# Kernel tuning notes

Hardware: AMD Instinct MI355X
Metric: run time of the kernel (lower is better)

Reference implementation:

```python
import jax, jax.numpy as jnp
import numpy as np

N = 4096          # residues (2 chains x 2048)
CHAINS = 2
LMAX = 2
L = (LMAX + 1) ** 2            # 9 spherical coefficients
BBC = 32                       # bb_channels
NBB = 3                        # n_bb_atoms - 1
SPH = BBC + NBB                # 35 sphere channels fed to attention
KNN = 20
LRK = 40
HEADS = 8
HC = 32
VC = HC // 4                   # attn_value_channels = 8
EDGE_F = 32                    # 16 RBF + 16 positional
L_IDX = np.repeat(np.arange(LMAX + 1), 2 * np.arange(LMAX + 1) + 1)  # degree of each of the 9 coeffs


def so3_linear(x, w, b):
    # x: [N,L,Cin]; w: [LMAX+1,Cin,Cout] shared across m within each degree l; bias only on l=0
    out = jnp.einsum('nlc,lcd->nld', x, w[L_IDX])
    return out.at[:, 0, :].add(b)


def _rbf(d):
    mu = jnp.linspace(0.0, 20.0, 16)
    sigma = 20.0 / 16
    return jnp.exp(-(((d[..., None] - mu) / sigma) ** 2))


def _edge_pos_embed(src, dst):
    d = (src - dst).astype(jnp.float32)
    freq = jnp.exp(jnp.arange(0, 16, 2, dtype=jnp.float32) * (-np.log(10000.0) / 16))
    ang = d[:, None] * freq
    return jnp.concatenate([jnp.cos(ang), jnp.sin(ang)], axis=-1)


def setup_inputs():
    key = jax.random.key(0)
    ks = jax.random.split(key, 16)
    n = lambda i, shp, s=1.0: jax.random.normal(ks[i], shp) * s
    return {
        'X_ca': n(0, (N, 3), 10.0),
        'bb_rel': n(1, (N, NBB, 3)),
        'bb_features': n(2, (N, L, BBC)),
        'batch': jnp.repeat(jnp.arange(CHAINS), N // CHAINS),
        'x_mask': jax.random.uniform(ks[3], (N,)) < 0.02,
        'noising_mask': jax.random.uniform(ks[4], (N,)) < 0.5,
        'attn_w1': n(5, (2 * SPH + EDGE_F, HC), 0.05), 'attn_b1': jnp.zeros((HC,)),
        'attn_w2': n(6, (HC, HEADS), 0.05), 'attn_b2': jnp.zeros((HEADS,)),
        'wv': n(7, (LMAX + 1, SPH, HEADS * VC), 0.05), 'bv': jnp.zeros((HEADS * VC,)),
        'wo': n(8, (LMAX + 1, HEADS * VC, BBC), 0.05), 'bo': jnp.zeros((BBC,)),
        'wg': n(9, (BBC, BBC), 0.05), 'bg': jnp.zeros((BBC,)),
        'wf': n(10, (LMAX + 1, BBC, BBC), 0.05), 'bf': jnp.zeros((BBC,)),
        'w_xca': n(11, (LMAX + 1, BBC, 1), 0.05), 'b_xca': jnp.zeros((1,)),
        'w_gate': n(12, (BBC, 1), 0.05), 'b_gate': jnp.zeros((1,)),
        'w_bb': n(13, (LMAX + 1, BBC, NBB), 0.05), 'b_bb': jnp.zeros((NBB,)),
    }


def reference(X_ca, bb_rel, bb_features, batch, x_mask, noising_mask,
              attn_w1, attn_b1, attn_w2, attn_b2, wv, bv, wo, bo, wg, bg, wf, bf,
              w_xca, b_xca, w_gate, b_gate, w_bb, b_bb):
    Nn = X_ca.shape[0]
    BIG = jnp.float32(1e30)
    # ---- graph construction (knn_graph + sample_inv_cubic_edges) ----
    x2 = jnp.sum(X_ca * X_ca, axis=-1)
    D2 = jnp.maximum(x2[:, None] + x2[None, :] - 2.0 * (X_ca @ X_ca.T), 0.0)  # [N,N]
    same = batch[:, None] == batch[None, :]
    eye = jnp.eye(Nn, dtype=bool)
    mask_pair = x_mask[:, None] | x_mask[None, :]
    invalid = (~same) | eye | mask_pair
    knn_idx = jax.lax.top_k(-jnp.where(invalid, BIG, D2), KNN)[1]   # [N,KNN] sources per target
    # long-range: inverse-cubic distance weights, Gumbel top-k sampling, excluding knn picks
    logits = jnp.where(invalid, -BIG, -1.5 * jnp.log(D2 + 1e-6))
    rows = jnp.arange(Nn)[:, None]
    logits = logits.at[rows, knn_idx].set(-BIG)
    gumb = jax.random.gumbel(jax.random.key(1), (Nn, Nn))
    lr_idx = jax.lax.top_k(logits + gumb, LRK)[1]                   # [N,LRK]
    src = jnp.concatenate([knn_idx.reshape(-1), lr_idx.reshape(-1)])
    dst = jnp.concatenate([jnp.repeat(jnp.arange(Nn), KNN), jnp.repeat(jnp.arange(Nn), LRK)])
    # ---- edge features: RBF(dist) + relative positional embedding ----
    dvec = X_ca[src] - X_ca[dst]
    dist = jnp.linalg.norm(dvec, axis=-1)
    edge_feat = jnp.concatenate([_rbf(dist), _edge_pos_embed(src, dst)], axis=-1)  # [M,32]
    # ---- assemble SO3 node embedding [N,L,35] ----
    node = jnp.zeros((Nn, L, SPH), X_ca.dtype)
    node = node.at[:, :, :BBC].set(bb_features)
    node = node.at[:, 1:4, BBC:].set(jnp.swapaxes(bb_rel, -1, -2))  # l=1 coeffs carry bb_rel
    node = node.at[:, 0, SPH - 1].set(noising_mask.astype(X_ca.dtype))
    # ---- equivariant graph attention (simplified TransBlockV2) ----
    inv = node[:, 0, :]                                             # invariant (l=0) features
    a_in = jnp.concatenate([inv[src], inv[dst], edge_feat], axis=-1)
    h = jax.nn.silu(a_in @ attn_w1 + attn_b1)
    logit = h @ attn_w2 + attn_b2                                   # [M,HEADS]
    mx = jax.ops.segment_max(logit, dst, num_segments=Nn)
    p = jnp.exp(logit - mx[dst])
    Z = jax.ops.segment_sum(p, dst, num_segments=Nn)
    alpha = p / (Z[dst] + 1e-9)                                     # segment softmax per target/head
    v = so3_linear(node, wv, bv)[src].reshape(-1, L, HEADS, VC)     # gather source values
    msg = (v * alpha[:, None, :, None]).reshape(-1, L, HEADS * VC)
    agg = jax.ops.segment_sum(msg, dst, num_segments=Nn)            # scatter to targets
    out = so3_linear(agg, wo, bo)                                   # [N,L,32]
    gate = jax.nn.silu(out[:, 0, :] @ wg + bg)                      # invariant-gated FFN
    out = out + so3_linear(out, wf, bf) * gate[:, None, :]
    # ---- coordinate / backbone updates ----
    upd_x = so3_linear(out, w_xca, b_xca)                           # [N,L,1]
    vec = upd_x[:, 1:4, 0]                                          # l=1 -> 3-vector
    g2 = jax.nn.softplus(out[:, 0, :] @ w_gate + b_gate)            # [N,1]
    new_X = X_ca + jnp.where(noising_mask[:, None], vec * g2, 0.0)
    upd_bb = so3_linear(out, w_bb, b_bb)                            # [N,L,3]
    dbb = jnp.swapaxes(upd_bb[:, 1:4, :], -1, -2)                   # [N,3,3]
    new_bb = bb_rel + jnp.where(noising_mask[:, None, None], dbb, 0.0)
    return new_X, new_bb, out
```

## Files before the change

kernel.cpp:

```cpp
#include <hip/hip_runtime.h>
#include <hip/hip_bf16.h>
#include <stdint.h>

#define NN 4096
#define CS 2048
#define KNN 20
#define LRK 40
#define EPN 60
#define NE (NN*EPN)
#define SPHC 35
#define BBCC 32
#define NHEAD 8
#define HVD 64
#define HCD 32
#define LT 9
#define MAXC 384

#define INVAL_D2 0xFFFFFFFEu
#define CONSUMED 0xFFFFFFFFu

__device__ __forceinline__ float fast_exp(float x) {
  return __builtin_amdgcn_exp2f(x * 1.4426950408889634f);
}
__device__ __forceinline__ float fast_cos(float a) {
  float rev = a * 0.15915494309189535f;
  rev = rev - __builtin_rintf(rev);
  return __builtin_amdgcn_cosf(rev);
}
__device__ __forceinline__ float fast_sin(float a) {
  float rev = a * 0.15915494309189535f;
  rev = rev - __builtin_rintf(rev);
  return __builtin_amdgcn_sinf(rev);
}

__device__ __forceinline__ float neglogu_f(int i, int j) {
  uint32_t c = ((uint32_t)(i & 2047) << 12) | (uint32_t)j;
  const uint32_t ks0 = 0u, ks1 = 1u, ks2 = 0x1BD11BDBu;
  uint32_t x0 = c + ks0;
  uint32_t x1 = (c + 0x800000u) + ks1;
#define TF_R(r) { x0 += x1; x1 = (x1 << (r)) | (x1 >> (32 - (r))); x1 ^= x0; }
  TF_R(13) TF_R(15) TF_R(26) TF_R(6)   x0 += ks1; x1 += ks2 + 1u;
  TF_R(17) TF_R(29) TF_R(16) TF_R(24)  x0 += ks2; x1 += ks0 + 2u;
  TF_R(13) TF_R(15) TF_R(26) TF_R(6)   x0 += ks0; x1 += ks1 + 3u;
  TF_R(17) TF_R(29) TF_R(16) TF_R(24)  x0 += ks1; x1 += ks2 + 4u;
  TF_R(13) TF_R(15) TF_R(26) TF_R(6)   x0 += ks2; x1 += ks0 + 5u;
#undef TF_R
  uint32_t b = (i >= 2048) ? x1 : x0;
  float u = __uint_as_float((b >> 9) | 0x3F800000u) - 1.0f;
  u = u + 1.17549435e-38f;
  return -logf(u);
}

__global__ void prep_kernel(const float* __restrict__ X,
                            const int* __restrict__ batch,
                            const int* __restrict__ xmask,
                            float4* __restrict__ Xw, uint32_t* __restrict__ bm) {
#pragma clang fp contract(off)
  int n = blockIdx.x * blockDim.x + threadIdx.x;
  if (n >= NN) return;
  float x = X[n*3+0], y = X[n*3+1], z = X[n*3+2];
  float x2 = (x*x + y*y) + z*z;
  Xw[n] = make_float4(x, y, z, x2);
  bm[n] = ((uint32_t)batch[n] << 1) | (xmask[n] ? 1u : 0u);
}

__global__ __launch_bounds__(256) void nodeproj_kernel(const float* __restrict__ bbf,
                                                       const int* __restrict__ nmask,
                                                       const float* __restrict__ w1,
                                                       const float* __restrict__ b1,
                                                       float* __restrict__ Pn,
                                                       float* __restrict__ Pd) {
  int tid = threadIdx.x;
  int t = tid & 31;
  int n = blockIdx.x * 8 + (tid >> 5);
  float bv_ = bbf[(size_t)n * (LT*BBCC) + t];
  float an = 0.f, ad = b1[t];
  #pragma unroll 8
  for (int c = 0; c < BBCC; c++) {
    float bc = __shfl(bv_, (tid & 32) + c, 64);
    an = fmaf(bc, w1[c * HCD + t], an);
    ad = fmaf(bc, w1[(SPHC + c) * HCD + t], ad);
  }
  float nm = nmask[n] ? 1.f : 0.f;
  an = fmaf(nm, w1[34 * HCD + t], an);
  ad = fmaf(nm, w1[69 * HCD + t], ad);
  Pn[n * HCD + t] = an;
  Pd[n * HCD + t] = ad;
}

__device__ __forceinline__ void sel2l(uint32_t* val, uint32_t* hist2,
                                      uint32_t* candk, uint32_t* candp,
                                      uint32_t* sh, int* sel,
                                      int k, int base, int cb, int tid) {
  {
    uint4* h4 = (uint4*)hist2;
    uint4 z; z.x = 0; z.y = 0; z.z = 0; z.w = 0;
    h4[tid] = z; h4[tid + 256] = z;
  }
  if (tid == 0) { sh[2] = 0; sh[3] = 0; }
  __syncthreads();
  #pragma unroll
  for (int q = 0; q < 8; q++) {
    uint32_t key = val[tid + (q << 8)];
    atomicAdd(&hist2[key >> 21], 1u);
  }
  __syncthreads();
  uint32_t h[8], s = 0;
  #pragma unroll
  for (int q = 0; q < 8; q++) { h[q] = hist2[tid*8 + q]; s += h[q]; }
  uint32_t cum = s;
  #pragma unroll
  for (int off = 1; off < 64; off <<= 1) {
    uint32_t o = __shfl_up(cum, off, 64);
    if ((tid & 63) >= off) cum += o;
  }
  if ((tid & 63) == 63) sh[8 + (tid >> 6)] = cum;
  __syncthreads();
  uint32_t woff = 0;
  for (int w = 0; w < (tid >> 6); w++) woff += sh[8 + w];
  uint32_t cumAll = cum + woff;
  uint32_t cumBefore = cumAll - s;
  uint32_t rk = (uint32_t)k;
  if (rk > cumBefore && rk <= cumAll) {
    uint32_t rloc = rk - cumBefore, lp = 0;
    bool done = false;
    #pragma unroll
    for (int q = 0; q < 8; q++) {
      lp += h[q];
      if (!done && rloc <= lp) { sh[0] = (uint32_t)(tid*8 + q); sh[1] = rloc - (lp - h[q]); done = true; }
    }
  }
  __syncthreads();
  const uint32_t B = sh[0], r = sh[1];
  #pragma unroll
  for (int q = 0; q < 8; q++) {
    int pos = tid + (q << 8);
    uint32_t key = val[pos];
    if ((key >> 21) == B) {
      uint32_t idx = atomicAdd(&sh[2], 1u);
      if (idx < MAXC) { candk[idx] = key; candp[idx] = (uint32_t)pos; }
    }
  }
  __syncthreads();
  int m = (int)sh[2]; if (m > MAXC) m = MAXC;
  if (tid < 64) {
    for (int ci = tid; ci < m; ci += 64) {
      unsigned long long k64 = ((unsigned long long)candk[ci] << 32) | candp[ci];
      uint32_t rank = 0;
      for (int j = 0; j < m; j++) {
        unsigned long long o = ((unsigned long long)candk[j] << 32) | candp[j];
        rank += (o < k64) ? 1u : 0u;
      }
      if (rank == r - 1) { sh[0] = candk[ci]; sh[1] = candp[ci]; }
    }
  }
  __syncthreads();
  const uint32_t vstar = sh[0], istar = sh[1];
  #pragma unroll
  for (int q = 0; q < 8; q++) {
    int pos = tid + (q << 8);
    uint32_t key = val[pos];
    if (key < vstar || (key == vstar && (uint32_t)pos <= istar)) {
      uint32_t slot = atomicAdd(&sh[3], 1u);
      sel[base + (int)slot] = cb + pos;
    }
  }
  __syncthreads();
}

__global__ __launch_bounds__(256) void select_kernel(const float4* __restrict__ Xw,
                                                     const uint32_t* __restrict__ bm,
                                                     int* __restrict__ srcO) {
#pragma clang fp contract(off)
  __shared__ uint32_t val[CS];
  __shared__ uint32_t hist2[2048];
  __shared__ uint32_t candk[MAXC];
  __shared__ uint32_t candp[MAXC];
  __shared__ uint32_t sh[12];
  __shared__ int sel[EPN];
  const int i = blockIdx.x, tid = threadIdx.x;
  const uint32_t bmi = bm[i];

  if (bmi & 1u) {
    if (tid < KNN) srcO[(size_t)i * EPN + tid] = tid;
    else if (tid < EPN) srcO[(size_t)i * EPN + tid] = tid - KNN;
    return;
  }
  const int cb = (int)(bmi >> 1) * CS;
  const float4 xi = Xw[i];

  #pragma unroll
  for (int q = 0; q < 8; q++) {
    int pos = tid + (q << 8);
    int j = cb + pos;
    float4 xj = Xw[j];
    uint32_t bmj = bm[j];
    bool inval = ((bmj & 1u) != 0u) || (j == i);
    float dot = xi.x*xj.x + xi.y*xj.y + xi.z*xj.z;
    float d2r = (xi.w + xj.w) - 2.0f*dot;
    float d2 = d2r > 0.0f ? d2r : 0.0f;
    val[pos] = inval ? INVAL_D2 : __float_as_uint(d2);
  }
  __syncthreads();

  sel2l(val, hist2, candk, candp, sh, sel, KNN, 0, cb, tid);

  if (tid < KNN) val[sel[tid] - cb] = CONSUMED;
  __syncthreads();

  #pragma unroll
  for (int q = 0; q < 8; q++) {
    int pos = tid + (q << 8);
    uint32_t v = val[pos];
    uint32_t skey;
    if (v >= INVAL_D2) skey = CONSUMED;
    else {
      float d2p = __uint_as_float(v) + 1e-6f;
      float w = d2p * sqrtf(d2p) * neglogu_f(i, cb + pos);
      skey = __float_as_uint(w);
    }
    val[pos] = skey;
  }
  __syncthreads();

  sel2l(val, hist2, candk, candp, sh, sel, LRK, KNN, cb, tid);

  if (tid < EPN) srcO[(size_t)i * EPN + tid] = sel[tid];
}

__global__ __launch_bounds__(256) void vmat_kernel(const float* __restrict__ bbf,
                                                   const float* __restrict__ bbrel,
                                                   const int* __restrict__ nmask,
                                                   const float* __restrict__ wv,
                                                   const float* __restrict__ bv,
                                                   float* __restrict__ V) {
  int row = blockIdx.x * 4 + (threadIdx.x >> 6);
  int d = threadIdx.x & 63;
  if (row >= NN * LT) return;
  int n = row / LT, l = row % LT;
  int li = (l == 0) ? 0 : (l < 4 ? 1 : 2);
  const float* w = wv + (size_t)li * SPHC * HVD;
  float acc = (l == 0) ? bv[d] : 0.f;
  const float* nb = bbf + (size_t)(n*LT + l) * BBCC;
  for (int c = 0; c < BBCC; c++) acc = fmaf(nb[c], w[c*HVD + d], acc);
  if (l >= 1 && l < 4) {
    for (int b = 0; b < 3; b++)
      acc = fmaf(bbrel[(size_t)(n*3 + b)*3 + (l-1)], w[(32+b)*HVD + d], acc);
  }
  if (l == 0) acc = fmaf(nmask[n] ? 1.f : 0.f, w[34*HVD + d], acc);
  V[(size_t)row * HVD + d] = acc;
}

__global__ __launch_bounds__(256) void edge_kernel(const int* __restrict__ src,
                                                   const float4* __restrict__ Xw,
                                                   const float* __restrict__ Pn,
                                                   const float* __restrict__ Pd,
                                                   const float* __restrict__ w1,
                                                   const float* __restrict__ w2,
                                                   const float* __restrict__ b2,
                                                   float* __restrict__ logitO) {
  const float FR[8] = {1.0f, 0.31622776601683794f, 0.1f, 0.031622776601683794f,
                       0.01f, 0.0031622776601683794f, 0.001f, 0.00031622776601683794f};
  __shared__ float w1cf[BBCC][HCD];
  __shared__ float w2f[HCD][NHEAD];
  __shared__ float b2f[NHEAD];
  __shared__ float ef[8][BBCC];
  __shared__ float hbuf[8][HCD];
  int tid = threadIdx.x;
  for (int q = tid; q < BBCC*HCD; q += 256) w1cf[q >> 5][q & 31] = w1[70*HCD + q];
  if (tid < HCD*NHEAD) w2f[tid >> 3][tid & 7] = w2[tid];
  if (tid < NHEAD) b2f[tid] = b2[tid];
  int sub = tid >> 5, t = tid & 31;
  int e = blockIdx.x * 8 + sub;
  int d = e / EPN;
  int s = src[e];
  float4 xs = Xw[s], xd = Xw[d];
  float dx = xs.x - xd.x, dy = xs.y - xd.y, dz = xs.z - xd.z;
  float dist = sqrtf(dx*dx + dy*dy + dz*dz);
  if (t < 16) {
    float mu = (20.0f / 15.0f) * (float)t;
    float zz = (dist - mu) / 1.25f;
    ef[sub][t] = fast_exp(-zz * zz);
  } else {
    int k = t - 16;
    float del = (float)(s - d);
    float a = del * FR[k & 7];
    ef[sub][t] = (k < 8) ? fast_cos(a) : fast_sin(a);
  }
  __syncthreads();
  float a = Pn[s * HCD + t] + Pd[d * HCD + t];
  #pragma unroll
  for (int k = 0; k < BBCC; k++) a = fmaf(ef[sub][k], w1cf[k][t], a);
  hbuf[sub][t] = a / (1.f + fast_exp(-a));
  __syncthreads();
  if (tid < 64) {
    int e2 = tid >> 3, hh = tid & 7;
    float lg = b2f[hh];
    #pragma unroll
    for (int c = 0; c < HCD; c++) lg = fmaf(hbuf[e2][c], w2f[c][hh], lg);
    logitO[(size_t)(blockIdx.x * 8 + e2) * NHEAD + hh] = lg;
  }
}

__global__ __launch_bounds__(64) void node_kernel(const int* __restrict__ src,
                                                  const float* __restrict__ logit,
                                                  const float* __restrict__ V,
                                                  const float* __restrict__ wo,
                                                  const float* __restrict__ bo,
                                                  const float* __restrict__ wg,
                                                  const float* __restrict__ bg,
                                                  const float* __restrict__ wf,
                                                  const float* __restrict__ bfb,
                                                  const float* __restrict__ w_xca,
                                                  const float* __restrict__ w_gate,
                                                  const float* __restrict__ b_gate,
                                                  const float* __restrict__ w_bb,
                                                  const float* __restrict__ X,
                                                  const float* __restrict__ bbrel,
                                                  const int* __restrict__ nmask,
                                                  float* __restrict__ out) {
  const int n = blockIdx.x, t = threadIdx.x;
  __shared__ float alpha[EPN][NHEAD];
  __shared__ int slist[EPN];
  __shared__ float agg[LT][HVD];
  __shared__ float o0[LT][BBCC];
  __shared__ float ofin[LT][BBCC];
  __shared__ float gate[BBCC];
  if (t < EPN) slist[t] = src[(size_t)n * EPN + t];
  for (int q = t; q < EPN * NHEAD; q += 64) alpha[q / NHEAD][q % NHEAD] = logit[(size_t)n * 480 + q];
  __syncthreads();
  if (t < NHEAD) {
    float m = -1e30f;
    for (int e = 0; e < EPN; e++) m = fmaxf(m, alpha[e][t]);
    float Z = 0.f;
    for (int e = 0; e < EPN; e++) { float p = expf(alpha[e][t] - m); alpha[e][t] = p; Z += p; }
    float iz = 1.f / (Z + 1e-9f);
    for (int e = 0; e < EPN; e++) alpha[e][t] *= iz;
  }
  __syncthreads();
  {
    const int h = t >> 3;
    float acc[LT];
    #pragma unroll
    for (int l = 0; l < LT; l++) acc[l] = 0.f;
    for (int e = 0; e < EPN; e++) {
      const float* Vp = V + (size_t)slist[e] * (LT * HVD) + t;
      float a = alpha[e][h];
      #pragma unroll
      for (int l = 0; l < LT; l++) acc[l] = fmaf(a, Vp[l * HVD], acc[l]);
    }
    #pragma unroll
    for (int l = 0; l < LT; l++) agg[l][t] = acc[l];
  }
  __syncthreads();
  for (int idx = t; idx < LT * BBCC; idx += 64) {
    int l = idx >> 5, d = idx & 31;
    int li = (l == 0) ? 0 : (l < 4 ? 1 : 2);
    float a = (l == 0) ? bo[d] : 0.f;
    const float* w = wo + (size_t)li * HVD * BBCC;
    for (int c = 0; c < HVD; c++) a = fmaf(agg[l][c], w[c * BBCC + d], a);
    o0[l][d] = a;
  }
  __syncthreads();
  if (t < BBCC) {
    float a = bg[t];
    for (int c = 0; c < BBCC; c++) a = fmaf(o0[0][c], wg[c * BBCC + t], a);
    gate[t] = a / (1.f + expf(-a));
  }
  __syncthreads();
  for (int idx = t; idx < LT * BBCC; idx += 64) {
    int l = idx >> 5, d = idx & 31;
    int li = (l == 0) ? 0 : (l < 4 ? 1 : 2);
    float a = (l == 0) ? bfb[d] : 0.f;
    const float* w = wf + (size_t)li * BBCC * BBCC;
    for (int c = 0; c < BBCC; c++) a = fmaf(o0[l][c], w[c * BBCC + d], a);
    float r = o0[l][d] + a * gate[d];
    ofin[l][d] = r;
    out[49152 + (size_t)n * 288 + idx] = r;
  }
  __syncthreads();
  float a2 = b_gate[0];
  for (int c = 0; c < BBCC; c++) a2 = fmaf(ofin[0][c], w_gate[c], a2);
  float g2 = fmaxf(a2, 0.f) + log1pf(expf(-fabsf(a2)));
  bool noise = nmask[n] != 0;
  if (t < 3) {
    float a = 0.f;
    for (int d2 = 0; d2 < BBCC; d2++) a = fmaf(ofin[1 + t][d2], w_xca[32 + d2], a);
    float nx = X[n * 3 + t] + (noise ? a * g2 : 0.f);
    out[(size_t)n * 3 + t] = nx;
  }
  if (t < 9) {
    int b = t / 3, c = t % 3;
    float a = 0.f;
    for (int d2 = 0; d2 < BBCC; d2++) a = fmaf(ofin[1 + c][d2], w_bb[(32 + d2) * 3 + b], a);
    float nb = bbrel[(size_t)(n * 3 + b) * 3 + c] + (noise ? a : 0.f);
    out[12288 + (size_t)n * 9 + b * 3 + c] = nb;
  }
}

extern "C" void kernel_launch(void* const* d_in, const int* in_sizes, int n_in,
                              void* d_out, int out_size, void* d_ws, size_t ws_size,
                              hipStream_t stream) {
  (void)in_sizes; (void)n_in; (void)out_size;
  const float* X      = (const float*)d_in[0];
  const float* bbrel  = (const float*)d_in[1];
  const float* bbf    = (const float*)d_in[2];
  const int* batch    = (const int*)d_in[3];
  const int* xmask    = (const int*)d_in[4];
  const int* nmask    = (const int*)d_in[5];
  const float* w1     = (const float*)d_in[6];
  const float* b1     = (const float*)d_in[7];
  const float* w2     = (const float*)d_in[8];
  const float* b2     = (const float*)d_in[9];
  const float* wv     = (const float*)d_in[10];
  const float* bv     = (const float*)d_in[11];
  const float* wo     = (const float*)d_in[12];
  const float* bo     = (const float*)d_in[13];
  const float* wg     = (const float*)d_in[14];
  const float* bg     = (const float*)d_in[15];
  const float* wf     = (const float*)d_in[16];
  const float* bfb    = (const float*)d_in[17];
  const float* w_xca  = (const float*)d_in[18];
  const float* w_gate = (const float*)d_in[20];
  const float* b_gate = (const float*)d_in[21];
  const float* w_bb   = (const float*)d_in[22];

  if (ws_size < 18939904) return;
  char* ws = (char*)d_ws;
  uint32_t* bmp   = (uint32_t*)(ws + 0);
  int*      srcl  = (int*)(ws + 16384);
  float*    logit = (float*)(ws + 999424);
  float*    V     = (float*)(ws + 8863744);
  float*    Pn    = (float*)(ws + 8863744);
  float*    Pd    = (float*)(ws + 9388032);
  float4*   Xw    = (float4*)(ws + 9912320);
  float*    out   = (float*)d_out;

  prep_kernel<<<NN / 256, 256, 0, stream>>>(X, batch, xmask, Xw, bmp);
  nodeproj_kernel<<<NN / 8, 256, 0, stream>>>(bbf, nmask, w1, b1, Pn, Pd);
  select_kernel<<<NN, 256, 0, stream>>>(Xw, bmp, srcl);
  edge_kernel<<<NE / 8, 256, 0, stream>>>(srcl, Xw, Pn, Pd, w1, w2, b2, logit);
  vmat_kernel<<<(NN * LT) / 4, 256, 0, stream>>>(bbf, bbrel, nmask, wv, bv, V);
  node_kernel<<<NN, 64, 0, stream>>>(srcl, logit, V, wo, bo, wg, bg, wf, bfb,
                                     w_xca, w_gate, b_gate, w_bb, X, bbrel, nmask, out);
}
```

Measured before the change: 271.8 us.

## Store V in bf16 and split node aggregation across four waves with LDS atomics

The value matrix V is written in bf16 instead of fp32, halving the bytes gathered per edge in the node kernel. The node kernel grows from one to four waves per node; each wave aggregates 15 of the 60 edges and the partial sums are combined with shared-memory atomic adds. The goal is more memory-level parallelism for the gather-bound aggregation and less traffic. In exchange, V loses precision in bf16 and the later per-node stages run on a larger block where most threads sit idle.

```diff
diff --git a/kernel.cpp b/kernel.cpp
--- a/kernel.cpp
+++ b/kernel.cpp
@@ -18,6 +18,8 @@
 
 #define INVAL_D2 0xFFFFFFFEu
 #define CONSUMED 0xFFFFFFFFu
+
+__device__ __forceinline__ float bf2f(__hip_bfloat16 x) { return __bfloat162float(x); }
 
 __device__ __forceinline__ float fast_exp(float x) {
   return __builtin_amdgcn_exp2f(x * 1.4426950408889634f);
@@ -233,7 +235,7 @@
                                                    const int* __restrict__ nmask,
                                                    const float* __restrict__ wv,
                                                    const float* __restrict__ bv,
-                                                   float* __restrict__ V) {
+                                                   __hip_bfloat16* __restrict__ V) {
   int row = blockIdx.x * 4 + (threadIdx.x >> 6);
   int d = threadIdx.x & 63;
   if (row >= NN * LT) return;
@@ -248,7 +250,7 @@
       acc = fmaf(bbrel[(size_t)(n*3 + b)*3 + (l-1)], w[(32+b)*HVD + d], acc);
   }
   if (l == 0) acc = fmaf(nmask[n] ? 1.f : 0.f, w[34*HVD + d], acc);
-  V[(size_t)row * HVD + d] = acc;
+  V[(size_t)row * HVD + d] = __float2bfloat16(acc);
 }
 
 __global__ __launch_bounds__(256) void edge_kernel(const int* __restrict__ src,
@@ -302,9 +304,9 @@
   }
 }
 
-__global__ __launch_bounds__(64) void node_kernel(const int* __restrict__ src,
+__global__ __launch_bounds__(256) void node_kernel(const int* __restrict__ src,
                                                   const float* __restrict__ logit,
-                                                  const float* __restrict__ V,
+                                                  const __hip_bfloat16* __restrict__ V,
                                                   const float* __restrict__ wo,
                                                   const float* __restrict__ bo,
                                                   const float* __restrict__ wg,
@@ -327,7 +329,15 @@
   __shared__ float ofin[LT][BBCC];
   __shared__ float gate[BBCC];
   if (t < EPN) slist[t] = src[(size_t)n * EPN + t];
-  for (int q = t; q < EPN * NHEAD; q += 64) alpha[q / NHEAD][q % NHEAD] = logit[(size_t)n * 480 + q];
+  if (t >= 64 && t < 64 + 2*EPN) {
+    int q = t - 64;
+    #pragma unroll
+    for (int z = 0; z < 4; z++) {
+      int idx = q * 4 + z;
+      alpha[idx >> 3][idx & 7] = logit[(size_t)n * 480 + idx];
+    }
+  }
+  for (int idx = t; idx < LT * HVD; idx += 256) agg[idx >> 6][idx & 63] = 0.f;
   __syncthreads();
   if (t < NHEAD) {
     float m = -1e30f;
@@ -339,21 +349,23 @@
   }
   __syncthreads();
   {
-    const int h = t >> 3;
+    const int wave = t >> 6, lane = t & 63;
+    const int h = lane >> 3;
     float acc[LT];
     #pragma unroll
     for (int l = 0; l < LT; l++) acc[l] = 0.f;
-    for (int e = 0; e < EPN; e++) {
-      const float* Vp = V + (size_t)slist[e] * (LT * HVD) + t;
+    const int e0 = wave * 15;
+    for (int e = e0; e < e0 + 15; e++) {
+      const __hip_bfloat16* Vp = V + (size_t)slist[e] * (LT * HVD) + lane;
       float a = alpha[e][h];
       #pragma unroll
-      for (int l = 0; l < LT; l++) acc[l] = fmaf(a, Vp[l * HVD], acc[l]);
+      for (int l = 0; l < LT; l++) acc[l] = fmaf(a, bf2f(Vp[l * HVD]), acc[l]);
     }
     #pragma unroll
-    for (int l = 0; l < LT; l++) agg[l][t] = acc[l];
-  }
-  __syncthreads();
-  for (int idx = t; idx < LT * BBCC; idx += 64) {
+    for (int l = 0; l < LT; l++) atomicAdd(&agg[l][lane], acc[l]);
+  }
+  __syncthreads();
+  for (int idx = t; idx < LT * BBCC; idx += 256) {
     int l = idx >> 5, d = idx & 31;
     int li = (l == 0) ? 0 : (l < 4 ? 1 : 2);
     float a = (l == 0) ? bo[d] : 0.f;
@@ -368,7 +380,7 @@
     gate[t] = a / (1.f + expf(-a));
   }
   __syncthreads();
-  for (int idx = t; idx < LT * BBCC; idx += 64) {
+  for (int idx = t; idx < LT * BBCC; idx += 256) {
     int l = idx >> 5, d = idx & 31;
     int li = (l == 0) ? 0 : (l < 4 ? 1 : 2);
     float a = (l == 0) ? bfb[d] : 0.f;
@@ -379,22 +391,24 @@
     out[49152 + (size_t)n * 288 + idx] = r;
   }
   __syncthreads();
-  float a2 = b_gate[0];
-  for (int c = 0; c < BBCC; c++) a2 = fmaf(ofin[0][c], w_gate[c], a2);
-  float g2 = fmaxf(a2, 0.f) + log1pf(expf(-fabsf(a2)));
-  bool noise = nmask[n] != 0;
-  if (t < 3) {
-    float a = 0.f;
-    for (int d2 = 0; d2 < BBCC; d2++) a = fmaf(ofin[1 + t][d2], w_xca[32 + d2], a);
-    float nx = X[n * 3 + t] + (noise ? a * g2 : 0.f);
-    out[(size_t)n * 3 + t] = nx;
-  }
-  if (t < 9) {
-    int b = t / 3, c = t % 3;
-    float a = 0.f;
-    for (int d2 = 0; d2 < BBCC; d2++) a = fmaf(ofin[1 + c][d2], w_bb[(32 + d2) * 3 + b], a);
-    float nb = bbrel[(size_t)(n * 3 + b) * 3 + c] + (noise ? a : 0.f);
-    out[12288 + (size_t)n * 9 + b * 3 + c] = nb;
+  if (t < 16) {
+    float a2 = b_gate[0];
+    for (int c = 0; c < BBCC; c++) a2 = fmaf(ofin[0][c], w_gate[c], a2);
+    float g2 = fmaxf(a2, 0.f) + log1pf(expf(-fabsf(a2)));
+    bool noise = nmask[n] != 0;
+    if (t < 3) {
+      float a = 0.f;
+      for (int d2 = 0; d2 < BBCC; d2++) a = fmaf(ofin[1 + t][d2], w_xca[32 + d2], a);
+      float nx = X[n * 3 + t] + (noise ? a * g2 : 0.f);
+      out[(size_t)n * 3 + t] = nx;
+    }
+    if (t < 9) {
+      int b = t / 3, c = t % 3;
+      float a = 0.f;
+      for (int d2 = 0; d2 < BBCC; d2++) a = fmaf(ofin[1 + c][d2], w_bb[(32 + d2) * 3 + b], a);
+      float nb = bbrel[(size_t)(n * 3 + b) * 3 + c] + (noise ? a : 0.f);
+      out[12288 + (size_t)n * 9 + b * 3 + c] = nb;
+    }
   }
 }
 
@@ -430,7 +444,7 @@
   uint32_t* bmp   = (uint32_t*)(ws + 0);
   int*      srcl  = (int*)(ws + 16384);
   float*    logit = (float*)(ws + 999424);
-  float*    V     = (float*)(ws + 8863744);
+  __hip_bfloat16* V = (__hip_bfloat16*)(ws + 8863744);
   float*    Pn    = (float*)(ws + 8863744);
   float*    Pd    = (float*)(ws + 9388032);
   float4*   Xw    = (float4*)(ws + 9912320);
@@ -441,6 +455,6 @@
   select_kernel<<<NN, 256, 0, stream>>>(Xw, bmp, srcl);
   edge_kernel<<<NE / 8, 256, 0, stream>>>(srcl, Xw, Pn, Pd, w1, w2, b2, logit);
   vmat_kernel<<<(NN * LT) / 4, 256, 0, stream>>>(bbf, bbrel, nmask, wv, bv, V);
-  node_kernel<<<NN, 64, 0, stream>>>(srcl, logit, V, wo, bo, wg, bg, wf, bfb,
-                                     w_xca, w_gate, b_gate, w_bb, X, bbrel, nmask, out);
-}
+  node_kernel<<<NN, 256, 0, stream>>>(srcl, logit, V, wo, bo, wg, bg, wf, bfb,
+                                      w_xca, w_gate, b_gate, w_bb, X, bbrel, nmask, out);
+}
```

New measurement: 323.0 us. 1.19x slower.
